# Performance work log

Measured on AMD Instinct MI355X. Metric: run time of the kernel, lower is better.

Reference implementation:

```python
import jax, jax.numpy as jnp
import numpy as np

EPS = 1e-5
N, F, D = 16384, 1024, 8


def setup_inputs() -> dict:
    key = jax.random.key(0)
    k1, k2, k3, k4 = jax.random.split(key, 4)
    x = jax.random.normal(k1, (N, F), dtype=jnp.float32)
    y = jax.random.randint(k2, (N,), 0, D, dtype=jnp.int64)
    # per-domain affine params (BatchNorm1d weight/bias per domain)
    gamma = 1.0 + 0.1 * jax.random.normal(k3, (D, F), dtype=jnp.float32)
    beta = 0.1 * jax.random.normal(k4, (D, F), dtype=jnp.float32)
    return {"x": x, "y": y, "gamma": gamma, "beta": beta}


def reference(x, y, gamma, beta):
    # Domain-specific batchnorm (training mode): per-domain batch stats,
    # biased variance, affine. Domains with 1 sample pass through x;
    # domains with 0 samples contribute nothing (out stays zero).
    d = gamma.shape[0]
    ones = jnp.ones((x.shape[0],), dtype=x.dtype)
    counts = jax.ops.segment_sum(ones, y, num_segments=d)          # [D]
    s1 = jax.ops.segment_sum(x, y, num_segments=d)                 # [D, F]
    s2 = jax.ops.segment_sum(x * x, y, num_segments=d)             # [D, F]
    cnt = jnp.maximum(counts, 1.0)[:, None]                        # avoid /0
    mean = s1 / cnt                                                # [D, F]
    var = s2 / cnt - mean * mean                                   # biased var
    inv = jax.lax.rsqrt(var + EPS)                                 # [D, F]
    xhat = (x - mean[y]) * inv[y]                                  # [N, F]
    out_bn = gamma[y] * xhat + beta[y]
    c = counts[y][:, None]                                         # [N, 1]
    return jnp.where(c > 1.0, out_bn, jnp.where(c == 1.0, x, jnp.zeros_like(x)))
```

## Files before the change

kernel.cpp:

```cpp
#include <hip/hip_runtime.h>


#define EPSV 1e-5f
constexpr int N = 16384;
constexpr int F = 1024;
constexpr int D = 8;
constexpr int ROWS_PER_BLOCK = 64;
constexpr int RG = N / ROWS_PER_BLOCK;

__global__ __launch_bounds__(256) void k1_partials(
    const float* __restrict__ x, const int* __restrict__ y,
    float* __restrict__ partials, int* __restrict__ counts) {
  const int t = threadIdx.x;
  const int rg = blockIdx.x >> 1;
  const int h = blockIdx.x & 1;

  __shared__ int hist[D];
  if (t < D) hist[t] = 0;
  __syncthreads();
  if (h == 0 && t < ROWS_PER_BLOCK) {
    int d = y[rg * ROWS_PER_BLOCK + t];
    atomicAdd(&hist[d], 1);
  }
  __syncthreads();
  if (h == 0 && t < D) atomicAdd(&counts[t], hist[t]);

  float2 a1[D], a2[D];
#pragma unroll
  for (int k = 0; k < D; ++k) {
    a1[k] = make_float2(0.f, 0.f);
    a2[k] = make_float2(0.f, 0.f);
  }

  const float2* __restrict__ x2 = (const float2*)x;
  const int col2 = h * 256 + t;
  const int row0 = rg * ROWS_PER_BLOCK;

#define ACC(K)                            \
  a1[K].x += v.x;                         \
  a1[K].y += v.y;                         \
  a2[K].x = fmaf(v.x, v.x, a2[K].x);      \
  a2[K].y = fmaf(v.y, v.y, a2[K].y);      \
  break;

  for (int r = 0; r < ROWS_PER_BLOCK; r += 8) {
    const int n = row0 + r;
    int dd[8];
    float2 vv[8];
#pragma unroll
    for (int j = 0; j < 8; ++j) dd[j] = y[n + j];
#pragma unroll
    for (int j = 0; j < 8; ++j) vv[j] = x2[(n + j) * 512 + col2];
#pragma unroll
    for (int j = 0; j < 8; ++j) {
      float2 v = vv[j];
      switch (dd[j]) {
        case 0: ACC(0)
        case 1: ACC(1)
        case 2: ACC(2)
        case 3: ACC(3)
        case 4: ACC(4)
        case 5: ACC(5)
        case 6: ACC(6)
        case 7: ACC(7)
      }
    }
  }
#undef ACC

  float4* __restrict__ p4 = (float4*)partials;
#pragma unroll
  for (int k = 0; k < D; ++k) {
    float4 w = make_float4(a1[k].x, a2[k].x, a1[k].y, a2[k].y);
    p4[(rg * D + k) * 512 + h * 256 + t] = w;
  }
}

__global__ __launch_bounds__(256) void k2_stats(
    const float* __restrict__ partials, const int* __restrict__ counts,
    const float* __restrict__ gamma, const float* __restrict__ beta,
    float* __restrict__ scale, float* __restrict__ shift) {
  const int p = blockIdx.x * 256 + threadIdx.x;
  const int d = p >> 10;

  const float2* __restrict__ pp = (const float2*)partials + p;
  float s1 = 0.f, s2 = 0.f;
#pragma unroll 8
  for (int rg = 0; rg < RG; ++rg) {
    float2 v = pp[rg * (D * F)];
    s1 += v.x;
    s2 += v.y;
  }

  const float c = (float)counts[d];
  const float cc = fmaxf(c, 1.f);
  const float mean = s1 / cc;
  const float var = s2 / cc - mean * mean;
  const float inv = rsqrtf(var + EPSV);
  float sc = gamma[p] * inv;
  float sh = beta[p] - mean * sc;
  if (c <= 1.f) {
    sc = (c == 1.f) ? 1.f : 0.f;
    sh = 0.f;
  }
  scale[p] = sc;
  shift[p] = sh;
}

__global__ __launch_bounds__(256) void k3_apply(
    const float* __restrict__ x, const int* __restrict__ y,
    const float* __restrict__ scale, const float* __restrict__ shift,
    float* __restrict__ out) {
  const int t = threadIdx.x;
  const int n0 = blockIdx.x * 8;

  int dd[8];
#pragma unroll
  for (int j = 0; j < 8; ++j) dd[j] = y[n0 + j];

#pragma unroll
  for (int j = 0; j < 8; ++j) {
    const int n = n0 + j;
    const float4 v = ((const float4*)x)[n * 256 + t];
    const float4 g = ((const float4*)scale)[dd[j] * 256 + t];
    const float4 b = ((const float4*)shift)[dd[j] * 256 + t];
    float4 o;
    o.x = fmaf(v.x, g.x, b.x);
    o.y = fmaf(v.y, g.y, b.y);
    o.z = fmaf(v.z, g.z, b.z);
    o.w = fmaf(v.w, g.w, b.w);
    ((float4*)out)[n * 256 + t] = o;
  }
}

extern "C" void kernel_launch(void* const* d_in, const int* in_sizes, int n_in,
                              void* d_out, int out_size, void* d_ws, size_t ws_size,
                              hipStream_t stream) {
  const float* x = (const float*)d_in[0];
  const int* y = (const int*)d_in[1];
  const float* gamma = (const float*)d_in[2];
  const float* beta = (const float*)d_in[3];
  float* out = (float*)d_out;

  float* partials = (float*)d_ws;
  const size_t poff = (size_t)RG * D * F * 2;
  int* counts = (int*)(partials + poff);
  float* scale = partials + poff + 64;
  float* shift = scale + D * F;

  hipMemsetAsync(counts, 0, D * sizeof(int), stream);
  k1_partials<<<RG * 2, 256, 0, stream>>>(x, y, partials, counts);
  k2_stats<<<(D * F) / 256, 256, 0, stream>>>(partials, counts, gamma, beta, scale, shift);
  k3_apply<<<N / 8, 256, 0, stream>>>(x, y, scale, shift, out);
}
```

Baseline: 149.0 us.

## Split partial-sum reduction into two stages and drop memset with per-block counts

The single k2 kernel, which ran only 32 blocks and had each thread serially sum 256 partials, is replaced by a 256-block first-stage reduction over groups of 16 row-groups and a small second-stage stats kernel. Per-block domain counts are now written to a buffer and reduced in shared memory, which removes the hipMemsetAsync and the global atomics. The goal is to fix the low parallelism and latency-bound reduction in the stats phase. The cost is an extra kernel launch and an intermediate buffer round trip.

```diff
diff --git a/kernel.cpp b/kernel.cpp
--- a/kernel.cpp
+++ b/kernel.cpp
@@ -10,7 +10,7 @@
 
 __global__ __launch_bounds__(256) void k1_partials(
     const float* __restrict__ x, const int* __restrict__ y,
-    float* __restrict__ partials, int* __restrict__ counts) {
+    float* __restrict__ partials, int* __restrict__ cnt_parts) {
   const int t = threadIdx.x;
   const int rg = blockIdx.x >> 1;
   const int h = blockIdx.x & 1;
@@ -23,7 +23,7 @@
     atomicAdd(&hist[d], 1);
   }
   __syncthreads();
-  if (h == 0 && t < D) atomicAdd(&counts[t], hist[t]);
+  if (h == 0 && t < D) cnt_parts[rg * D + t] = hist[t];
 
   float2 a1[D], a2[D];
 #pragma unroll
@@ -76,35 +76,59 @@
   }
 }
 
-__global__ __launch_bounds__(256) void k2_stats(
-    const float* __restrict__ partials, const int* __restrict__ counts,
+__global__ __launch_bounds__(256) void k2a_reduce(
+    const float4* __restrict__ partials, float4* __restrict__ out16) {
+  const int rgg = blockIdx.x >> 4;
+  const int q = blockIdx.x & 15;
+  const int idx = q * 256 + threadIdx.x;
+  const float4* __restrict__ p = partials + (size_t)(rgg * 16) * 4096 + idx;
+  float4 s = make_float4(0.f, 0.f, 0.f, 0.f);
+#pragma unroll
+  for (int i = 0; i < 16; ++i) {
+    float4 v = p[i * 4096];
+    s.x += v.x; s.y += v.y; s.z += v.z; s.w += v.w;
+  }
+  out16[rgg * 4096 + idx] = s;
+}
+
+__global__ __launch_bounds__(256) void k2b_stats(
+    const float* __restrict__ out16, const int* __restrict__ cnt_parts,
     const float* __restrict__ gamma, const float* __restrict__ beta,
     float* __restrict__ scale, float* __restrict__ shift) {
-  const int p = blockIdx.x * 256 + threadIdx.x;
+  const int t = threadIdx.x;
+  const int p = blockIdx.x * 256 + t;
   const int d = p >> 10;
 
-  const float2* __restrict__ pp = (const float2*)partials + p;
+  __shared__ int sc[256];
+  sc[t] = cnt_parts[t * D + d];
+  __syncthreads();
+  for (int s = 128; s > 0; s >>= 1) {
+    if (t < s) sc[t] += sc[t + s];
+    __syncthreads();
+  }
+  const float c = (float)sc[0];
+
+  const float2* __restrict__ pp = (const float2*)out16 + p;
   float s1 = 0.f, s2 = 0.f;
-#pragma unroll 8
-  for (int rg = 0; rg < RG; ++rg) {
-    float2 v = pp[rg * (D * F)];
+#pragma unroll
+  for (int i = 0; i < 16; ++i) {
+    float2 v = pp[i * (D * F)];
     s1 += v.x;
     s2 += v.y;
   }
 
-  const float c = (float)counts[d];
   const float cc = fmaxf(c, 1.f);
   const float mean = s1 / cc;
   const float var = s2 / cc - mean * mean;
   const float inv = rsqrtf(var + EPSV);
-  float sc = gamma[p] * inv;
-  float sh = beta[p] - mean * sc;
+  float scv = gamma[p] * inv;
+  float shv = beta[p] - mean * scv;
   if (c <= 1.f) {
-    sc = (c == 1.f) ? 1.f : 0.f;
-    sh = 0.f;
+    scv = (c == 1.f) ? 1.f : 0.f;
+    shv = 0.f;
   }
-  scale[p] = sc;
-  shift[p] = sh;
+  scale[p] = scv;
+  shift[p] = shv;
 }
 
 __global__ __launch_bounds__(256) void k3_apply(
@@ -143,13 +167,13 @@
   float* out = (float*)d_out;
 
   float* partials = (float*)d_ws;
-  const size_t poff = (size_t)RG * D * F * 2;
-  int* counts = (int*)(partials + poff);
-  float* scale = partials + poff + 64;
+  float* out16 = partials + (size_t)RG * D * F * 2;
+  int* cnt_parts = (int*)(out16 + 16 * D * F * 2);
+  float* scale = (float*)(cnt_parts + RG * D);
   float* shift = scale + D * F;
 
-  hipMemsetAsync(counts, 0, D * sizeof(int), stream);
-  k1_partials<<<RG * 2, 256, 0, stream>>>(x, y, partials, counts);
-  k2_stats<<<(D * F) / 256, 256, 0, stream>>>(partials, counts, gamma, beta, scale, shift);
+  k1_partials<<<RG * 2, 256, 0, stream>>>(x, y, partials, cnt_parts);
+  k2a_reduce<<<256, 256, 0, stream>>>((const float4*)partials, (float4*)out16);
+  k2b_stats<<<32, 256, 0, stream>>>(out16, cnt_parts, gamma, beta, scale, shift);
   k3_apply<<<N / 8, 256, 0, stream>>>(x, y, scale, shift, out);
 }
```

New measurement: 138.2 us. 7.2% less time.
